# Optimization experiments

Hardware: AMD Instinct MI355X
Metric: run time of the kernel (lower is better)

The kernel has to match this reference:

```python
import jax, jax.numpy as jnp
import numpy as np


def setup_inputs() -> dict:
    key = jax.random.key(0)
    k1, k2, k3 = jax.random.split(key, 3)
    B, L, D = 2, 8192, 1024
    x = jax.random.normal(k1, (B, L, D), dtype=jnp.float32)
    h = jax.random.normal(k2, (L, D), dtype=jnp.float32)
    bias = jax.random.normal(k3, (D,), dtype=jnp.float32) * 0.02
    return {"x": x, "h": h, "bias": bias}


def reference(x, h, bias):
    # x: (B, L, D), h: (filter_len, D), bias: (D,)
    B, L, D = x.shape
    filter_len = h.shape[0]
    # next power of two >= L + filter_len - 1 (static, from shapes)
    fft_size = 1 << int(L + filter_len - 1).bit_length()
    x_f = jnp.fft.rfft(x, n=fft_size, axis=1)          # (B, fft_size//2+1, D) complex
    h_f = jnp.fft.rfft(h, n=fft_size, axis=0)          # (fft_size//2+1, D) complex
    y = jnp.fft.irfft(x_f * h_f[None, :, :], n=fft_size, axis=1)
    y = y[:, :L, :]                                    # causal-length truncation
    return y + bias
```

## Files before the change

### kernel.cpp

```cpp
#include <hip/hip_runtime.h>

#define D_CH   1024
#define L_SEQ  8192
#define NCH    32
#define W_N    3.8349519697141029e-4f
#define W128A  4.90873852123405e-2f

__device__ __forceinline__ float bf2f(unsigned v){
  union { float f; unsigned u; } x; x.u = v << 16;
  return x.f;
}
__device__ __forceinline__ unsigned packc(float r, float i){
  unsigned u;
  asm("v_cvt_pk_bf16_f32 %0, %1, %2" : "=v"(u) : "v"(r), "v"(i));
  return u;
}
__device__ __forceinline__ float2 upk(unsigned u){
  return make_float2(bf2f(u & 0xffffu), bf2f(u >> 16));
}

__device__ __host__ constexpr int bitrev4(int j){
  return ((j&1)<<3)|((j&2)<<1)|((j&4)>>1)|((j&8)>>3);
}
__device__ __host__ constexpr int bitrev3(int j){
  return ((j&1)<<2)|(j&2)|((j&4)>>2);
}

template<int SGN>
__device__ __forceinline__ void dft16(float2* x){
  const float TC[8] = {1.f, 0.9238795325f, 0.7071067812f, 0.3826834324f,
                       0.f, -0.3826834324f, -0.7071067812f, -0.9238795325f};
  const float TS[8] = {0.f, -0.3826834324f, -0.7071067812f, -0.9238795325f,
                       -1.f, -0.9238795325f, -0.7071067812f, -0.3826834324f};
#pragma unroll
  for (int len = 16; len >= 2; len >>= 1){
    const int half = len >> 1, tstep = 16 / len;
#pragma unroll
    for (int st = 0; st < 16; st += len){
#pragma unroll
      for (int j = 0; j < half; j++){
        const float wr = TC[j*tstep];
        const float wi = (SGN > 0) ? TS[j*tstep] : -TS[j*tstep];
        const int a = st + j, b = a + half;
        const float ur = x[a].x, ui = x[a].y;
        const float vr = x[b].x, vi = x[b].y;
        x[a].x = ur + vr; x[a].y = ui + vi;
        const float dr = ur - vr, di = ui - vi;
        x[b].x = dr*wr - di*wi;
        x[b].y = dr*wi + di*wr;
      }
    }
  }
}

template<int SGN>
__device__ __forceinline__ void dft8(float2* x){
  const float TC[4] = {1.f, 0.7071067812f, 0.f, -0.7071067812f};
  const float TS[4] = {0.f, -0.7071067812f, -1.f, -0.7071067812f};
#pragma unroll
  for (int len = 8; len >= 2; len >>= 1){
    const int half = len >> 1, tstep = 8 / len;
#pragma unroll
    for (int st = 0; st < 8; st += len){
#pragma unroll
      for (int j = 0; j < half; j++){
        const float wr = TC[j*tstep];
        const float wi = (SGN > 0) ? TS[j*tstep] : -TS[j*tstep];
        const int a = st + j, b = a + half;
        const float ur = x[a].x, ui = x[a].y;
        const float vr = x[b].x, vi = x[b].y;
        x[a].x = ur + vr; x[a].y = ui + vi;
        const float dr = ur - vr, di = ui - vi;
        x[b].x = dr*wr - di*wi;
        x[b].y = dr*wi + di*wr;
      }
    }
  }
}

__device__ __forceinline__ void build_twF(float2* twF, int tid){
  if (tid < 128){
    const int pp = tid >> 4, kk = tid & 15;
    float sn, cs;
    __sincosf(-W128A * (float)(pp * kk), &sn, &cs);
    twF[tid] = make_float2(cs, sn);
  }
}

template<int SGN>
__device__ __forceinline__ void fft128(float2* v, float2* lds,
                                       const float2* twF, int ch, int p){
  dft16<SGN>(v);
#pragma unroll
  for (int slot = 0; slot < 8; slot++){
    const int r = bitrev3(slot);
    const float2 t = twF[p*16 + 2*r];
    const float cs = t.x;
    const float sn = (SGN > 0) ? t.y : -t.y;
    const float2 a = v[slot];
    lds[(p*8 + r)*NCH + ch] = make_float2(a.x*cs - a.y*sn, a.x*sn + a.y*cs);
  }
  __syncthreads();
  float2 t8[8];
#pragma unroll
  for (int pp = 0; pp < 8; pp++) t8[pp] = lds[(pp*8 + p)*NCH + ch];
  dft8<SGN>(t8);
#pragma unroll
  for (int t = 0; t < 8; t++) v[t] = t8[t];
  __syncthreads();
#pragma unroll
  for (int slot = 8; slot < 16; slot++){
    const int r = bitrev3(slot - 8);
    const float2 t = twF[p*16 + 2*r + 1];
    const float cs = t.x;
    const float sn = (SGN > 0) ? t.y : -t.y;
    const float2 a = v[slot];
    lds[(p*8 + r)*NCH + ch] = make_float2(a.x*cs - a.y*sn, a.x*sn + a.y*cs);
  }
  __syncthreads();
#pragma unroll
  for (int pp = 0; pp < 8; pp++) t8[pp] = lds[(pp*8 + p)*NCH + ch];
  dft8<SGN>(t8);
#pragma unroll
  for (int t = 0; t < 8; t++) v[8 + t] = t8[t];
}

__global__ __launch_bounds__(256, 8)
void k1_step1(const float* __restrict__ x, const float* __restrict__ h,
              unsigned* __restrict__ Az, unsigned* __restrict__ Ah){
  __shared__ float2 lds[64*NCH];
  __shared__ float2 twF[128];
  __shared__ float2 twO[128];
  const int n2 = blockIdx.x, dg = blockIdx.y, mode = blockIdx.z;
  const int tid = threadIdx.x;
  const int ch = tid & (NCH-1), p = tid >> 5;
  const int d = dg*NCH + ch;

  build_twF(twF, tid);
  if (tid >= 128 && tid < 256){
    const int k1v = tid - 128;
    float sn, cs;
    __sincosf(-W_N * (float)(k1v * n2), &sn, &cs);
    twO[k1v] = make_float2(cs, sn);
  }

  float2 v[16];
  if (mode == 0){
    const float* x0 = x;
    const float* x1 = x + (size_t)L_SEQ * D_CH;
#pragma unroll
    for (int q = 0; q < 8; q++){
      const size_t off = (size_t)(n2 + 128*(p + 8*q)) * D_CH + d;
      v[q] = make_float2(x0[off], x1[off]);
    }
  } else {
#pragma unroll
    for (int q = 0; q < 8; q++){
      const size_t off = (size_t)(n2 + 128*(p + 8*q)) * D_CH + d;
      v[q] = make_float2(h[off], 0.0f);
    }
  }
#pragma unroll
  for (int q = 8; q < 16; q++) v[q] = make_float2(0.f, 0.f);

  __syncthreads();
  fft128<1>(v, lds, twF, ch, p);

  unsigned* __restrict__ A = mode ? Ah : Az;
#pragma unroll
  for (int c = 0; c < 2; c++){
#pragma unroll
    for (int t = 0; t < 8; t++){
      const int k1v = (2*p + c) + 16*bitrev3(t);
      const float2 w = twO[k1v];
      const float2 a = v[c*8 + t];
      A[((size_t)k1v*128 + n2)*D_CH + d] =
        packc(a.x*w.x - a.y*w.y, a.x*w.y + a.y*w.x);
    }
  }
}

__global__ __launch_bounds__(256, 4)
void k2_zh(unsigned* __restrict__ Az, const unsigned* __restrict__ Ah){
  __shared__ float2 lds[64*NCH];
  __shared__ float2 twF[128];
  const int k1 = blockIdx.x, dg = blockIdx.y;
  const int tid = threadIdx.x;
  const int ch = tid & (NCH-1), p = tid >> 5;
  const int d = dg*NCH + ch;
  const size_t base = (size_t)k1 * 128 * D_CH + d;

  build_twF(twF, tid);

  unsigned ha[16], za[16];
#pragma unroll
  for (int q = 0; q < 16; q++)
    ha[q] = Ah[base + (size_t)(p + 8*q) * D_CH];
#pragma unroll
  for (int q = 0; q < 16; q++)
    za[q] = Az[base + (size_t)(p + 8*q) * D_CH];

  __syncthreads();

  float2 v[16];
#pragma unroll
  for (int q = 0; q < 16; q++) v[q] = upk(ha[q]);
  fft128<1>(v, lds, twF, ch, p);
  unsigned hs[16];
  const float sc = 1.0f / 16384.0f;
#pragma unroll
  for (int i = 0; i < 16; i++) hs[i] = packc(v[i].x * sc, v[i].y * sc);
  __syncthreads();

#pragma unroll
  for (int q = 0; q < 16; q++) v[q] = upk(za[q]);
  fft128<1>(v, lds, twF, ch, p);

#pragma unroll
  for (int i = 0; i < 16; i++){
    const float2 hv = upk(hs[i]);
    const float zr = v[i].x, zi = v[i].y;
    v[i] = make_float2(zr*hv.x - zi*hv.y, zr*hv.y + zi*hv.x);
  }

  __syncthreads();
  float2 w[8];
#pragma unroll
  for (int c = 0; c < 2; c++)
#pragma unroll
    for (int t = 0; t < 8; t += 2){
      const int k2 = (2*p + c) + 16*bitrev3(t);
      lds[k2*NCH + ch] = v[c*8 + t];
    }
  __syncthreads();
#pragma unroll
  for (int q = 0; q < 8; q++) w[q] = lds[(p + 8*q)*NCH + ch];
  __syncthreads();
#pragma unroll
  for (int c = 0; c < 2; c++)
#pragma unroll
    for (int t = 1; t < 8; t += 2){
      const int k2 = (2*p + c) + 16*bitrev3(t) - 64;
      lds[k2*NCH + ch] = v[c*8 + t];
    }
  __syncthreads();
#pragma unroll
  for (int q = 0; q < 8; q++) v[8 + q] = lds[(p + 8*q)*NCH + ch];
  __syncthreads();
#pragma unroll
  for (int q = 0; q < 8; q++) v[q] = w[q];

  fft128<-1>(v, lds, twF, ch, p);

#pragma unroll
  for (int c = 0; c < 2; c++){
#pragma unroll
    for (int t = 0; t < 8; t++){
      const int m2 = (2*p + c) + 16*bitrev3(t);
      const float2 a = v[c*8 + t];
      Az[base + (size_t)m2 * D_CH] = packc(a.x, a.y);
    }
  }
}

__global__ __launch_bounds__(256, 6)
void k3_inv2(const unsigned* __restrict__ Bz, const float* __restrict__ bias,
             float* __restrict__ out){
  __shared__ float2 lds[64*NCH];
  __shared__ float2 twF[128];
  __shared__ float2 twI[128];
  const int m2 = blockIdx.x, dg = blockIdx.y;
  const int tid = threadIdx.x;
  const int ch = tid & (NCH-1), p = tid >> 5;
  const int d = dg*NCH + ch;
  const float bv = bias[d];

  build_twF(twF, tid);
  if (tid >= 128 && tid < 256){
    const int k1 = tid - 128;
    float sn, cs;
    __sincosf(W_N * (float)(m2 * k1), &sn, &cs);
    twI[k1] = make_float2(cs, sn);
  }

  unsigned raw[16];
#pragma unroll
  for (int q = 0; q < 16; q++){
    const int k1 = p + 8*q;
    raw[q] = Bz[((size_t)k1*128 + m2) * D_CH + d];
  }

  __syncthreads();

  float2 v[16];
#pragma unroll
  for (int q = 0; q < 16; q++){
    const float2 w = twI[p + 8*q];
    const float2 a = upk(raw[q]);
    v[q] = make_float2(a.x*w.x - a.y*w.y, a.x*w.y + a.y*w.x);
  }

  fft128<-1>(v, lds, twF, ch, p);

#pragma unroll
  for (int c = 0; c < 2; c++){
#pragma unroll
    for (int t = 0; t < 8; t += 2){
      const int m1 = (2*p + c) + 16*bitrev3(t);
      const int tseq = m2 + 128*m1;
      const float2 a = v[c*8 + t];
      out[(size_t)tseq * D_CH + d]            = a.x + bv;
      out[(size_t)(L_SEQ + tseq) * D_CH + d]  = a.y + bv;
    }
  }
}

extern "C" void kernel_launch(void* const* d_in, const int* in_sizes, int n_in,
                              void* d_out, int out_size, void* d_ws, size_t ws_size,
                              hipStream_t stream){
  (void)in_sizes; (void)n_in; (void)out_size;
  const float* x    = (const float*)d_in[0];
  const float* h    = (const float*)d_in[1];
  const float* bias = (const float*)d_in[2];
  float* out = (float*)d_out;

  const size_t REGION = (size_t)128 * 128 * D_CH * sizeof(unsigned);
  unsigned *r1, *r2;
  if (ws_size >= 2 * REGION){
    r1 = (unsigned*)d_ws;
    r2 = (unsigned*)((char*)d_ws + REGION);
  } else {
    r1 = (unsigned*)d_out;
    r2 = (unsigned*)d_ws;
  }

  const dim3 blk(256, 1, 1);
  hipLaunchKernelGGL(k1_step1, dim3(128,32,2), blk, 0, stream, x, h, r1, r2);
  hipLaunchKernelGGL(k2_zh,    dim3(128,32,1), blk, 0, stream, r1, r2);
  hipLaunchKernelGGL(k3_inv2,  dim3(128,32,1), blk, 0, stream, r1, bias, out);
}
```

Measured before the change: 235.3 us.

## Process two channels per thread in forward and inverse FFT kernels

k1 and k3 now handle two adjacent channels per thread, using float4 registers, 8-byte global loads and stores, and a float4 LDS transpose buffer. The grid along the channel dimension is halved and launch bounds drop to 4 blocks per SM. The aim is wider memory transactions and twiddle reuse across two channels. In exchange, register and LDS use per block roughly double, which lowers occupancy.

After: 236.7 us. About the same (+0.6%).

```diff
diff --git a/kernel.cpp b/kernel.cpp
--- a/kernel.cpp
+++ b/kernel.cpp
@@ -17,6 +17,14 @@
 }
 __device__ __forceinline__ float2 upk(unsigned u){
   return make_float2(bf2f(u & 0xffffu), bf2f(u >> 16));
+}
+__device__ __forceinline__ float4 upk2(uint2 u){
+  return make_float4(bf2f(u.x & 0xffffu), bf2f(u.x >> 16),
+                     bf2f(u.y & 0xffffu), bf2f(u.y >> 16));
+}
+__device__ __forceinline__ float4 cmul2(float4 a, float cs, float sn){
+  return make_float4(a.x*cs - a.y*sn, a.x*sn + a.y*cs,
+                     a.z*cs - a.w*sn, a.z*sn + a.w*cs);
 }
 
 __device__ __host__ constexpr int bitrev4(int j){
@@ -78,6 +86,56 @@
   }
 }
 
+template<int SGN>
+__device__ __forceinline__ void dft16v4(float4* x){
+  const float TC[8] = {1.f, 0.9238795325f, 0.7071067812f, 0.3826834324f,
+                       0.f, -0.3826834324f, -0.7071067812f, -0.9238795325f};
+  const float TS[8] = {0.f, -0.3826834324f, -0.7071067812f, -0.9238795325f,
+                       -1.f, -0.9238795325f, -0.7071067812f, -0.3826834324f};
+#pragma unroll
+  for (int len = 16; len >= 2; len >>= 1){
+    const int half = len >> 1, tstep = 16 / len;
+#pragma unroll
+    for (int st = 0; st < 16; st += len){
+#pragma unroll
+      for (int j = 0; j < half; j++){
+        const float wr = TC[j*tstep];
+        const float wi = (SGN > 0) ? TS[j*tstep] : -TS[j*tstep];
+        const int a = st + j, b = a + half;
+        const float4 u = x[a], v = x[b];
+        x[a] = make_float4(u.x+v.x, u.y+v.y, u.z+v.z, u.w+v.w);
+        const float4 dd = make_float4(u.x-v.x, u.y-v.y, u.z-v.z, u.w-v.w);
+        x[b] = make_float4(dd.x*wr - dd.y*wi, dd.x*wi + dd.y*wr,
+                           dd.z*wr - dd.w*wi, dd.z*wi + dd.w*wr);
+      }
+    }
+  }
+}
+
+template<int SGN>
+__device__ __forceinline__ void dft8v4(float4* x){
+  const float TC[4] = {1.f, 0.7071067812f, 0.f, -0.7071067812f};
+  const float TS[4] = {0.f, -0.7071067812f, -1.f, -0.7071067812f};
+#pragma unroll
+  for (int len = 8; len >= 2; len >>= 1){
+    const int half = len >> 1, tstep = 8 / len;
+#pragma unroll
+    for (int st = 0; st < 8; st += len){
+#pragma unroll
+      for (int j = 0; j < half; j++){
+        const float wr = TC[j*tstep];
+        const float wi = (SGN > 0) ? TS[j*tstep] : -TS[j*tstep];
+        const int a = st + j, b = a + half;
+        const float4 u = x[a], v = x[b];
+        x[a] = make_float4(u.x+v.x, u.y+v.y, u.z+v.z, u.w+v.w);
+        const float4 dd = make_float4(u.x-v.x, u.y-v.y, u.z-v.z, u.w-v.w);
+        x[b] = make_float4(dd.x*wr - dd.y*wi, dd.x*wi + dd.y*wr,
+                           dd.z*wr - dd.w*wi, dd.z*wi + dd.w*wr);
+      }
+    }
+  }
+}
+
 __device__ __forceinline__ void build_twF(float2* twF, int tid){
   if (tid < 128){
     const int pp = tid >> 4, kk = tid & 15;
@@ -125,16 +183,52 @@
   for (int t = 0; t < 8; t++) v[8 + t] = t8[t];
 }
 
-__global__ __launch_bounds__(256, 8)
+template<int SGN>
+__device__ __forceinline__ void fft128v4(float4* v, float4* lds4,
+                                         const float2* twF, int ch, int p){
+  dft16v4<SGN>(v);
+#pragma unroll
+  for (int slot = 0; slot < 8; slot++){
+    const int r = bitrev3(slot);
+    const float2 t = twF[p*16 + 2*r];
+    const float cs = t.x;
+    const float sn = (SGN > 0) ? t.y : -t.y;
+    lds4[(p*8 + r)*32 + ch] = cmul2(v[slot], cs, sn);
+  }
+  __syncthreads();
+  float4 t8[8];
+#pragma unroll
+  for (int pp = 0; pp < 8; pp++) t8[pp] = lds4[(pp*8 + p)*32 + ch];
+  dft8v4<SGN>(t8);
+#pragma unroll
+  for (int t = 0; t < 8; t++) v[t] = t8[t];
+  __syncthreads();
+#pragma unroll
+  for (int slot = 8; slot < 16; slot++){
+    const int r = bitrev3(slot - 8);
+    const float2 t = twF[p*16 + 2*r + 1];
+    const float cs = t.x;
+    const float sn = (SGN > 0) ? t.y : -t.y;
+    lds4[(p*8 + r)*32 + ch] = cmul2(v[slot], cs, sn);
+  }
+  __syncthreads();
+#pragma unroll
+  for (int pp = 0; pp < 8; pp++) t8[pp] = lds4[(pp*8 + p)*32 + ch];
+  dft8v4<SGN>(t8);
+#pragma unroll
+  for (int t = 0; t < 8; t++) v[8 + t] = t8[t];
+}
+
+__global__ __launch_bounds__(256, 4)
 void k1_step1(const float* __restrict__ x, const float* __restrict__ h,
               unsigned* __restrict__ Az, unsigned* __restrict__ Ah){
-  __shared__ float2 lds[64*NCH];
+  __shared__ float4 lds4[64*32];
   __shared__ float2 twF[128];
   __shared__ float2 twO[128];
   const int n2 = blockIdx.x, dg = blockIdx.y, mode = blockIdx.z;
   const int tid = threadIdx.x;
-  const int ch = tid & (NCH-1), p = tid >> 5;
-  const int d = dg*NCH + ch;
+  const int ch = tid & 31, p = tid >> 5;
+  const int d = dg*64 + 2*ch;
 
   build_twF(twF, tid);
   if (tid >= 128 && tid < 256){
@@ -144,27 +238,30 @@
     twO[k1v] = make_float2(cs, sn);
   }
 
-  float2 v[16];
+  float4 v[16];
   if (mode == 0){
     const float* x0 = x;
     const float* x1 = x + (size_t)L_SEQ * D_CH;
 #pragma unroll
     for (int q = 0; q < 8; q++){
       const size_t off = (size_t)(n2 + 128*(p + 8*q)) * D_CH + d;
-      v[q] = make_float2(x0[off], x1[off]);
+      const float2 a = *(const float2*)(x0 + off);
+      const float2 b = *(const float2*)(x1 + off);
+      v[q] = make_float4(a.x, b.x, a.y, b.y);
     }
   } else {
 #pragma unroll
     for (int q = 0; q < 8; q++){
       const size_t off = (size_t)(n2 + 128*(p + 8*q)) * D_CH + d;
-      v[q] = make_float2(h[off], 0.0f);
-    }
-  }
-#pragma unroll
-  for (int q = 8; q < 16; q++) v[q] = make_float2(0.f, 0.f);
-
-  __syncthreads();
-  fft128<1>(v, lds, twF, ch, p);
+      const float2 a = *(const float2*)(h + off);
+      v[q] = make_float4(a.x, 0.f, a.y, 0.f);
+    }
+  }
+#pragma unroll
+  for (int q = 8; q < 16; q++) v[q] = make_float4(0.f, 0.f, 0.f, 0.f);
+
+  __syncthreads();
+  fft128v4<1>(v, lds4, twF, ch, p);
 
   unsigned* __restrict__ A = mode ? Ah : Az;
 #pragma unroll
@@ -173,9 +270,9 @@
     for (int t = 0; t < 8; t++){
       const int k1v = (2*p + c) + 16*bitrev3(t);
       const float2 w = twO[k1v];
-      const float2 a = v[c*8 + t];
-      A[((size_t)k1v*128 + n2)*D_CH + d] =
-        packc(a.x*w.x - a.y*w.y, a.x*w.y + a.y*w.x);
+      const float4 r = cmul2(v[c*8 + t], w.x, w.y);
+      *(uint2*)&A[((size_t)k1v*128 + n2)*D_CH + d] =
+        make_uint2(packc(r.x, r.y), packc(r.z, r.w));
     }
   }
 }
@@ -263,17 +360,17 @@
   }
 }
 
-__global__ __launch_bounds__(256, 6)
+__global__ __launch_bounds__(256, 4)
 void k3_inv2(const unsigned* __restrict__ Bz, const float* __restrict__ bias,
              float* __restrict__ out){
-  __shared__ float2 lds[64*NCH];
+  __shared__ float4 lds4[64*32];
   __shared__ float2 twF[128];
   __shared__ float2 twI[128];
   const int m2 = blockIdx.x, dg = blockIdx.y;
   const int tid = threadIdx.x;
-  const int ch = tid & (NCH-1), p = tid >> 5;
-  const int d = dg*NCH + ch;
-  const float bv = bias[d];
+  const int ch = tid & 31, p = tid >> 5;
+  const int d = dg*64 + 2*ch;
+  const float2 bv = *(const float2*)(bias + d);
 
   build_twF(twF, tid);
   if (tid >= 128 && tid < 256){
@@ -283,24 +380,23 @@
     twI[k1] = make_float2(cs, sn);
   }
 
-  unsigned raw[16];
+  uint2 raw[16];
 #pragma unroll
   for (int q = 0; q < 16; q++){
     const int k1 = p + 8*q;
-    raw[q] = Bz[((size_t)k1*128 + m2) * D_CH + d];
-  }
-
-  __syncthreads();
-
-  float2 v[16];
+    raw[q] = *(const uint2*)&Bz[((size_t)k1*128 + m2) * D_CH + d];
+  }
+
+  __syncthreads();
+
+  float4 v[16];
 #pragma unroll
   for (int q = 0; q < 16; q++){
     const float2 w = twI[p + 8*q];
-    const float2 a = upk(raw[q]);
-    v[q] = make_float2(a.x*w.x - a.y*w.y, a.x*w.y + a.y*w.x);
-  }
-
-  fft128<-1>(v, lds, twF, ch, p);
+    v[q] = cmul2(upk2(raw[q]), w.x, w.y);
+  }
+
+  fft128v4<-1>(v, lds4, twF, ch, p);
 
 #pragma unroll
   for (int c = 0; c < 2; c++){
@@ -308,9 +404,11 @@
     for (int t = 0; t < 8; t += 2){
       const int m1 = (2*p + c) + 16*bitrev3(t);
       const int tseq = m2 + 128*m1;
-      const float2 a = v[c*8 + t];
-      out[(size_t)tseq * D_CH + d]            = a.x + bv;
-      out[(size_t)(L_SEQ + tseq) * D_CH + d]  = a.y + bv;
+      const float4 a = v[c*8 + t];
+      *(float2*)&out[(size_t)tseq * D_CH + d] =
+        make_float2(a.x + bv.x, a.z + bv.y);
+      *(float2*)&out[(size_t)(L_SEQ + tseq) * D_CH + d] =
+        make_float2(a.y + bv.x, a.w + bv.y);
     }
   }
 }
@@ -335,7 +433,7 @@
   }
 
   const dim3 blk(256, 1, 1);
-  hipLaunchKernelGGL(k1_step1, dim3(128,32,2), blk, 0, stream, x, h, r1, r2);
+  hipLaunchKernelGGL(k1_step1, dim3(128,16,2), blk, 0, stream, x, h, r1, r2);
   hipLaunchKernelGGL(k2_zh,    dim3(128,32,1), blk, 0, stream, r1, r2);
-  hipLaunchKernelGGL(k3_inv2,  dim3(128,32,1), blk, 0, stream, r1, bias, out);
-}
+  hipLaunchKernelGGL(k3_inv2,  dim3(128,16,1), blk, 0, stream, r1, bias, out);
+}
```

## Exploit real-filter Hermitian symmetry, zero-padding DFT16, and two columns per block

Applied to the files above, without the earlier changes.

The first-stage FFT now uses a specialized radix-16 that skips the butterflies whose upper half is zero padding. For the real filter h, only the first half of the step-1 outputs is written, and k2 rebuilds the rest from Hermitian symmetry plus a twiddle. k1 and k3 now process two n2/m2 columns per block with separate LDS buffers, halving the grid and overlapping loads across two FFTs. This trades more registers and LDS, with fewer blocks per CU, for less arithmetic and memory traffic.

New measurement: 232.8 us. No clear change (-1.0%).

```diff
diff --git a/kernel.cpp b/kernel.cpp
--- a/kernel.cpp
+++ b/kernel.cpp
@@ -19,9 +19,6 @@
   return make_float2(bf2f(u & 0xffffu), bf2f(u >> 16));
 }
 
-__device__ __host__ constexpr int bitrev4(int j){
-  return ((j&1)<<3)|((j&2)<<1)|((j&4)>>1)|((j&8)>>3);
-}
 __device__ __host__ constexpr int bitrev3(int j){
   return ((j&1)<<2)|(j&2)|((j&4)>>2);
 }
@@ -54,14 +51,24 @@
 }
 
 template<int SGN>
-__device__ __forceinline__ void dft8(float2* x){
-  const float TC[4] = {1.f, 0.7071067812f, 0.f, -0.7071067812f};
-  const float TS[4] = {0.f, -0.7071067812f, -1.f, -0.7071067812f};
+__device__ __forceinline__ void dft16z(float2* x){
+  const float TC[8] = {1.f, 0.9238795325f, 0.7071067812f, 0.3826834324f,
+                       0.f, -0.3826834324f, -0.7071067812f, -0.9238795325f};
+  const float TS[8] = {0.f, -0.3826834324f, -0.7071067812f, -0.9238795325f,
+                       -1.f, -0.9238795325f, -0.7071067812f, -0.3826834324f};
+#pragma unroll
+  for (int j = 0; j < 8; j++){
+    const float wr = TC[j];
+    const float wi = (SGN > 0) ? TS[j] : -TS[j];
+    const float ur = x[j].x, ui = x[j].y;
+    x[j+8].x = ur*wr - ui*wi;
+    x[j+8].y = ur*wi + ui*wr;
+  }
 #pragma unroll
   for (int len = 8; len >= 2; len >>= 1){
-    const int half = len >> 1, tstep = 8 / len;
-#pragma unroll
-    for (int st = 0; st < 8; st += len){
+    const int half = len >> 1, tstep = 16 / len;
+#pragma unroll
+    for (int st = 0; st < 16; st += len){
 #pragma unroll
       for (int j = 0; j < half; j++){
         const float wr = TC[j*tstep];
@@ -78,6 +85,31 @@
   }
 }
 
+template<int SGN>
+__device__ __forceinline__ void dft8(float2* x){
+  const float TC[4] = {1.f, 0.7071067812f, 0.f, -0.7071067812f};
+  const float TS[4] = {0.f, -0.7071067812f, -1.f, -0.7071067812f};
+#pragma unroll
+  for (int len = 8; len >= 2; len >>= 1){
+    const int half = len >> 1, tstep = 8 / len;
+#pragma unroll
+    for (int st = 0; st < 8; st += len){
+#pragma unroll
+      for (int j = 0; j < half; j++){
+        const float wr = TC[j*tstep];
+        const float wi = (SGN > 0) ? TS[j*tstep] : -TS[j*tstep];
+        const int a = st + j, b = a + half;
+        const float ur = x[a].x, ui = x[a].y;
+        const float vr = x[b].x, vi = x[b].y;
+        x[a].x = ur + vr; x[a].y = ui + vi;
+        const float dr = ur - vr, di = ui - vi;
+        x[b].x = dr*wr - di*wi;
+        x[b].y = dr*wi + di*wr;
+      }
+    }
+  }
+}
+
 __device__ __forceinline__ void build_twF(float2* twF, int tid){
   if (tid < 128){
     const int pp = tid >> 4, kk = tid & 15;
@@ -87,10 +119,10 @@
   }
 }
 
-template<int SGN>
+template<int SGN, bool ZT>
 __device__ __forceinline__ void fft128(float2* v, float2* lds,
                                        const float2* twF, int ch, int p){
-  dft16<SGN>(v);
+  if (ZT) dft16z<SGN>(v); else dft16<SGN>(v);
 #pragma unroll
   for (int slot = 0; slot < 8; slot++){
     const int r = bitrev3(slot);
@@ -125,56 +157,78 @@
   for (int t = 0; t < 8; t++) v[8 + t] = t8[t];
 }
 
-__global__ __launch_bounds__(256, 8)
+__global__ __launch_bounds__(256, 4)
 void k1_step1(const float* __restrict__ x, const float* __restrict__ h,
               unsigned* __restrict__ Az, unsigned* __restrict__ Ah){
-  __shared__ float2 lds[64*NCH];
+  __shared__ float2 ldsA[64*NCH];
+  __shared__ float2 ldsB[64*NCH];
   __shared__ float2 twF[128];
-  __shared__ float2 twO[128];
-  const int n2 = blockIdx.x, dg = blockIdx.y, mode = blockIdx.z;
+  __shared__ float2 twOa[128];
+  __shared__ float2 twOb[128];
+  const int n2a = blockIdx.x*2, n2b = n2a + 1;
+  const int dg = blockIdx.y, mode = blockIdx.z;
   const int tid = threadIdx.x;
   const int ch = tid & (NCH-1), p = tid >> 5;
   const int d = dg*NCH + ch;
 
-  build_twF(twF, tid);
-  if (tid >= 128 && tid < 256){
-    const int k1v = tid - 128;
-    float sn, cs;
-    __sincosf(-W_N * (float)(k1v * n2), &sn, &cs);
-    twO[k1v] = make_float2(cs, sn);
-  }
-
-  float2 v[16];
+  float2 va[16], vb[16];
   if (mode == 0){
     const float* x0 = x;
     const float* x1 = x + (size_t)L_SEQ * D_CH;
 #pragma unroll
     for (int q = 0; q < 8; q++){
-      const size_t off = (size_t)(n2 + 128*(p + 8*q)) * D_CH + d;
-      v[q] = make_float2(x0[off], x1[off]);
+      const size_t ra = (size_t)(n2a + 128*(p + 8*q)) * D_CH + d;
+      const size_t rb = (size_t)(n2b + 128*(p + 8*q)) * D_CH + d;
+      va[q] = make_float2(x0[ra], x1[ra]);
+      vb[q] = make_float2(x0[rb], x1[rb]);
     }
   } else {
 #pragma unroll
     for (int q = 0; q < 8; q++){
-      const size_t off = (size_t)(n2 + 128*(p + 8*q)) * D_CH + d;
-      v[q] = make_float2(h[off], 0.0f);
-    }
-  }
-#pragma unroll
-  for (int q = 8; q < 16; q++) v[q] = make_float2(0.f, 0.f);
-
-  __syncthreads();
-  fft128<1>(v, lds, twF, ch, p);
+      const size_t ra = (size_t)(n2a + 128*(p + 8*q)) * D_CH + d;
+      const size_t rb = (size_t)(n2b + 128*(p + 8*q)) * D_CH + d;
+      va[q] = make_float2(h[ra], 0.f);
+      vb[q] = make_float2(h[rb], 0.f);
+    }
+  }
+
+  build_twF(twF, tid);
+  if (tid >= 128){
+    const int k1v = tid - 128;
+    float sn, cs;
+    __sincosf(-W_N * (float)(k1v * n2a), &sn, &cs);
+    twOa[k1v] = make_float2(cs, sn);
+    __sincosf(-W_N * (float)(k1v * n2b), &sn, &cs);
+    twOb[k1v] = make_float2(cs, sn);
+  }
+  __syncthreads();
 
   unsigned* __restrict__ A = mode ? Ah : Az;
+
+  fft128<1, true>(va, ldsA, twF, ch, p);
 #pragma unroll
   for (int c = 0; c < 2; c++){
 #pragma unroll
     for (int t = 0; t < 8; t++){
       const int k1v = (2*p + c) + 16*bitrev3(t);
-      const float2 w = twO[k1v];
-      const float2 a = v[c*8 + t];
-      A[((size_t)k1v*128 + n2)*D_CH + d] =
+      if (mode == 1 && k1v > 64) continue;
+      const float2 w = twOa[k1v];
+      const float2 a = va[c*8 + t];
+      A[((size_t)k1v*128 + n2a)*D_CH + d] =
+        packc(a.x*w.x - a.y*w.y, a.x*w.y + a.y*w.x);
+    }
+  }
+
+  fft128<1, true>(vb, ldsB, twF, ch, p);
+#pragma unroll
+  for (int c = 0; c < 2; c++){
+#pragma unroll
+    for (int t = 0; t < 8; t++){
+      const int k1v = (2*p + c) + 16*bitrev3(t);
+      if (mode == 1 && k1v > 64) continue;
+      const float2 w = twOb[k1v];
+      const float2 a = vb[c*8 + t];
+      A[((size_t)k1v*128 + n2b)*D_CH + d] =
         packc(a.x*w.x - a.y*w.y, a.x*w.y + a.y*w.x);
     }
   }
@@ -184,28 +238,45 @@
 void k2_zh(unsigned* __restrict__ Az, const unsigned* __restrict__ Ah){
   __shared__ float2 lds[64*NCH];
   __shared__ float2 twF[128];
+  __shared__ float2 tw1[128];
   const int k1 = blockIdx.x, dg = blockIdx.y;
   const int tid = threadIdx.x;
   const int ch = tid & (NCH-1), p = tid >> 5;
   const int d = dg*NCH + ch;
-  const size_t base = (size_t)k1 * 128 * D_CH + d;
+  const int k1r = (k1 > 64) ? 128 - k1 : k1;
+  const size_t basez = (size_t)k1  * 128 * D_CH + d;
+  const size_t baseh = (size_t)k1r * 128 * D_CH + d;
 
   build_twF(twF, tid);
+  if (tid < 128){
+    float sn, cs;
+    __sincosf(-W128A * (float)tid, &sn, &cs);
+    tw1[tid] = make_float2(cs, sn);
+  }
 
   unsigned ha[16], za[16];
 #pragma unroll
   for (int q = 0; q < 16; q++)
-    ha[q] = Ah[base + (size_t)(p + 8*q) * D_CH];
+    ha[q] = Ah[baseh + (size_t)(p + 8*q) * D_CH];
 #pragma unroll
   for (int q = 0; q < 16; q++)
-    za[q] = Az[base + (size_t)(p + 8*q) * D_CH];
+    za[q] = Az[basez + (size_t)(p + 8*q) * D_CH];
 
   __syncthreads();
 
   float2 v[16];
-#pragma unroll
-  for (int q = 0; q < 16; q++) v[q] = upk(ha[q]);
-  fft128<1>(v, lds, twF, ch, p);
+  if (k1 <= 64){
+#pragma unroll
+    for (int q = 0; q < 16; q++) v[q] = upk(ha[q]);
+  } else {
+#pragma unroll
+    for (int q = 0; q < 16; q++){
+      const float2 a = upk(ha[q]);
+      const float2 t = tw1[p + 8*q];
+      v[q] = make_float2(t.x*a.x + t.y*a.y, t.y*a.x - t.x*a.y);
+    }
+  }
+  fft128<1, false>(v, lds, twF, ch, p);
   unsigned hs[16];
   const float sc = 1.0f / 16384.0f;
 #pragma unroll
@@ -214,7 +285,7 @@
 
 #pragma unroll
   for (int q = 0; q < 16; q++) v[q] = upk(za[q]);
-  fft128<1>(v, lds, twF, ch, p);
+  fft128<1, false>(v, lds, twF, ch, p);
 
 #pragma unroll
   for (int i = 0; i < 16; i++){
@@ -250,7 +321,7 @@
 #pragma unroll
   for (int q = 0; q < 8; q++) v[q] = w[q];
 
-  fft128<-1>(v, lds, twF, ch, p);
+  fft128<-1, false>(v, lds, twF, ch, p);
 
 #pragma unroll
   for (int c = 0; c < 2; c++){
@@ -258,56 +329,78 @@
     for (int t = 0; t < 8; t++){
       const int m2 = (2*p + c) + 16*bitrev3(t);
       const float2 a = v[c*8 + t];
-      Az[base + (size_t)m2 * D_CH] = packc(a.x, a.y);
-    }
-  }
-}
-
-__global__ __launch_bounds__(256, 6)
+      Az[basez + (size_t)m2 * D_CH] = packc(a.x, a.y);
+    }
+  }
+}
+
+__global__ __launch_bounds__(256, 4)
 void k3_inv2(const unsigned* __restrict__ Bz, const float* __restrict__ bias,
              float* __restrict__ out){
-  __shared__ float2 lds[64*NCH];
+  __shared__ float2 ldsA[64*NCH];
+  __shared__ float2 ldsB[64*NCH];
   __shared__ float2 twF[128];
-  __shared__ float2 twI[128];
-  const int m2 = blockIdx.x, dg = blockIdx.y;
+  __shared__ float2 twIa[128];
+  __shared__ float2 twIb[128];
+  const int m2a = blockIdx.x*2, m2b = m2a + 1;
+  const int dg = blockIdx.y;
   const int tid = threadIdx.x;
   const int ch = tid & (NCH-1), p = tid >> 5;
   const int d = dg*NCH + ch;
   const float bv = bias[d];
 
+  unsigned rawa[16], rawb[16];
+#pragma unroll
+  for (int q = 0; q < 16; q++){
+    const int k1 = p + 8*q;
+    rawa[q] = Bz[((size_t)k1*128 + m2a) * D_CH + d];
+    rawb[q] = Bz[((size_t)k1*128 + m2b) * D_CH + d];
+  }
+
   build_twF(twF, tid);
-  if (tid >= 128 && tid < 256){
+  if (tid >= 128){
     const int k1 = tid - 128;
     float sn, cs;
-    __sincosf(W_N * (float)(m2 * k1), &sn, &cs);
-    twI[k1] = make_float2(cs, sn);
-  }
-
-  unsigned raw[16];
+    __sincosf(W_N * (float)(m2a * k1), &sn, &cs);
+    twIa[k1] = make_float2(cs, sn);
+    __sincosf(W_N * (float)(m2b * k1), &sn, &cs);
+    twIb[k1] = make_float2(cs, sn);
+  }
+  __syncthreads();
+
+  float2 v[16];
 #pragma unroll
   for (int q = 0; q < 16; q++){
-    const int k1 = p + 8*q;
-    raw[q] = Bz[((size_t)k1*128 + m2) * D_CH + d];
-  }
-
-  __syncthreads();
-
-  float2 v[16];
-#pragma unroll
-  for (int q = 0; q < 16; q++){
-    const float2 w = twI[p + 8*q];
-    const float2 a = upk(raw[q]);
+    const float2 w = twIa[p + 8*q];
+    const float2 a = upk(rawa[q]);
     v[q] = make_float2(a.x*w.x - a.y*w.y, a.x*w.y + a.y*w.x);
   }
-
-  fft128<-1>(v, lds, twF, ch, p);
-
+  fft128<-1, false>(v, ldsA, twF, ch, p);
 #pragma unroll
   for (int c = 0; c < 2; c++){
 #pragma unroll
     for (int t = 0; t < 8; t += 2){
       const int m1 = (2*p + c) + 16*bitrev3(t);
-      const int tseq = m2 + 128*m1;
+      const int tseq = m2a + 128*m1;
+      const float2 a = v[c*8 + t];
+      out[(size_t)tseq * D_CH + d]            = a.x + bv;
+      out[(size_t)(L_SEQ + tseq) * D_CH + d]  = a.y + bv;
+    }
+  }
+
+#pragma unroll
+  for (int q = 0; q < 16; q++){
+    const float2 w = twIb[p + 8*q];
+    const float2 a = upk(rawb[q]);
+    v[q] = make_float2(a.x*w.x - a.y*w.y, a.x*w.y + a.y*w.x);
+  }
+  fft128<-1, false>(v, ldsB, twF, ch, p);
+#pragma unroll
+  for (int c = 0; c < 2; c++){
+#pragma unroll
+    for (int t = 0; t < 8; t += 2){
+      const int m1 = (2*p + c) + 16*bitrev3(t);
+      const int tseq = m2b + 128*m1;
       const float2 a = v[c*8 + t];
       out[(size_t)tseq * D_CH + d]            = a.x + bv;
       out[(size_t)(L_SEQ + tseq) * D_CH + d]  = a.y + bv;
@@ -335,7 +428,7 @@
   }
 
   const dim3 blk(256, 1, 1);
-  hipLaunchKernelGGL(k1_step1, dim3(128,32,2), blk, 0, stream, x, h, r1, r2);
+  hipLaunchKernelGGL(k1_step1, dim3(64,32,2), blk, 0, stream, x, h, r1, r2);
   hipLaunchKernelGGL(k2_zh,    dim3(128,32,1), blk, 0, stream, r1, r2);
-  hipLaunchKernelGGL(k3_inv2,  dim3(128,32,1), blk, 0, stream, r1, bias, out);
-}
+  hipLaunchKernelGGL(k3_inv2,  dim3(64,32,1), blk, 0, stream, r1, bias, out);
+}
```
